# Kernel tuning notes

Measured on AMD Instinct MI355X. Metric: run time of the kernel, lower is better.

The kernel has to match this reference:

```python
import jax, jax.numpy as jnp
import numpy as np

S = 7               # grid size (config.S)
LAMBDA_COORD = 5.0  # YOLOv1 coordinate loss weight
LAMBDA_NOOBJ = 0.5  # YOLOv1 no-object confidence weight
BATCH = 16384


def _iou(a, b):
    """IoU of boxes in (cx, cy, w, h) format. a, b: [..., 4] -> [...]."""
    a_lt = a[..., 0:2] - a[..., 2:4] * 0.5
    a_rb = a[..., 0:2] + a[..., 2:4] * 0.5
    b_lt = b[..., 0:2] - b[..., 2:4] * 0.5
    b_rb = b[..., 0:2] + b[..., 2:4] * 0.5
    inter_wh = jnp.clip(jnp.minimum(a_rb, b_rb) - jnp.maximum(a_lt, b_lt), 0.0)
    inter = inter_wh[..., 0] * inter_wh[..., 1]
    area_a = a[..., 2] * a[..., 3]
    area_b = b[..., 2] * b[..., 3]
    return inter / (area_a + area_b - inter + 1e-10)


def setup_inputs() -> dict:
    key = jax.random.key(0)
    k1, k2, k3 = jax.random.split(key, 3)
    preds = jax.random.uniform(k1, (BATCH, S, S, 30), dtype=jnp.float32)
    labels = jax.random.uniform(k2, (BATCH, S, S, 30), dtype=jnp.float32)
    # objectness flag must be exactly 1.0 in object cells (labels[...,4]==1 check)
    conf = (jax.random.uniform(k3, (BATCH, S, S, 1)) > 0.7).astype(jnp.float32)
    labels = labels.at[..., 4:5].set(conf)
    labels = labels.at[..., 9:10].set(conf)
    return {"preds": preds, "labels": labels}


def _yolo_loss(preds, labels):
    obj = labels[..., 4]          # [B,S,S] 1.0 where an object is present
    noobj = 1.0 - obj
    gt = labels[..., 0:4]         # ground-truth box per cell
    p1 = preds[..., 0:4]          # bbox 1
    p2 = preds[..., 5:9]          # bbox 2

    iou1 = _iou(p1, gt)
    iou2 = _iou(p2, gt)
    resp1 = (iou1 > iou2).astype(preds.dtype)  # responsible-box selector
    r1 = resp1[..., None]

    resp_box = r1 * p1 + (1.0 - r1) * p2
    resp_conf = resp1 * preds[..., 4] + (1.0 - resp1) * preds[..., 9]
    other_conf = (1.0 - resp1) * preds[..., 4] + resp1 * preds[..., 9]
    resp_iou = jax.lax.stop_gradient(jnp.maximum(iou1, iou2))  # conf target

    om = obj[..., None]
    loss_xy = LAMBDA_COORD * jnp.sum(om * (resp_box[..., 0:2] - gt[..., 0:2]) ** 2)
    sqrt_p = jnp.sqrt(jnp.maximum(resp_box[..., 2:4], 1e-8))
    sqrt_g = jnp.sqrt(jnp.maximum(gt[..., 2:4], 1e-8))
    loss_wh = LAMBDA_COORD * jnp.sum(om * (sqrt_p - sqrt_g) ** 2)
    loss_obj = jnp.sum(obj * (resp_conf - resp_iou) ** 2)
    loss_noobj = LAMBDA_NOOBJ * (
        jnp.sum(noobj * (preds[..., 4] ** 2 + preds[..., 9] ** 2))
        + jnp.sum(obj * other_conf ** 2)
    )
    loss_cls = jnp.sum(om * (preds[..., 10:] - labels[..., 10:]) ** 2)

    total = loss_xy + loss_wh + loss_obj + loss_noobj + loss_cls
    return total / preds.shape[0]


def reference(preds, labels):
    return _yolo_loss(preds, labels)
```

## Files before the change

kernel.cpp:

```cpp
#include <hip/hip_runtime.h>

#define NCELLS (16384 * 7 * 7)
#define THREADS 256
#define TILE_CELLS 256
#define FLOATS_PER_TILE (TILE_CELLS * 30)
#define NTILES (NCELLS / TILE_CELLS)
#define GRID 256

__device__ __forceinline__ void gload16(const float* g, float* l) {
    __builtin_amdgcn_global_load_lds(
        (const __attribute__((address_space(1))) void*)g,
        (__attribute__((address_space(3))) void*)l, 16, 0, 0);
}

__device__ __forceinline__ void stage_tile(const float* __restrict__ preds,
                                           const float* __restrict__ labels,
                                           float* sp, float* sl,
                                           int tile, int wid, int lane) {
    size_t base = (size_t)tile * FLOATS_PER_TILE;
    #pragma unroll
    for (int k = 0; k < 15; ++k) {
        int c = wid * 15 + k;
        if (c < 30) {
            gload16(preds + base + (size_t)c * 256 + lane * 4, sp + c * 256);
        } else {
            int c2 = c - 30;
            gload16(labels + base + (size_t)c2 * 256 + lane * 4, sl + c2 * 256);
        }
    }
}

__device__ __forceinline__ float cell_loss(const float* p, const float* l) {
    float g_l = l[0] - l[2] * 0.5f, g_r = l[0] + l[2] * 0.5f;
    float g_t = l[1] - l[3] * 0.5f, g_b = l[1] + l[3] * 0.5f;
    float area_g = l[2] * l[3];

    float a_l = p[0] - p[2] * 0.5f, a_r = p[0] + p[2] * 0.5f;
    float a_t = p[1] - p[3] * 0.5f, a_b = p[1] + p[3] * 0.5f;
    float iw1 = fmaxf(fminf(a_r, g_r) - fmaxf(a_l, g_l), 0.0f);
    float ih1 = fmaxf(fminf(a_b, g_b) - fmaxf(a_t, g_t), 0.0f);
    float inter1 = iw1 * ih1;
    float iou1 = inter1 / (p[2] * p[3] + area_g - inter1 + 1e-10f);

    float b_l = p[5] - p[7] * 0.5f, b_r = p[5] + p[7] * 0.5f;
    float b_t = p[6] - p[8] * 0.5f, b_b = p[6] + p[8] * 0.5f;
    float iw2 = fmaxf(fminf(b_r, g_r) - fmaxf(b_l, g_l), 0.0f);
    float ih2 = fmaxf(fminf(b_b, g_b) - fmaxf(b_t, g_t), 0.0f);
    float inter2 = iw2 * ih2;
    float iou2 = inter2 / (p[7] * p[8] + area_g - inter2 + 1e-10f);

    bool r1 = iou1 > iou2;
    float rb0 = r1 ? p[0] : p[5];
    float rb1 = r1 ? p[1] : p[6];
    float rb2 = r1 ? p[2] : p[7];
    float rb3 = r1 ? p[3] : p[8];
    float rconf = r1 ? p[4] : p[9];
    float oconf = r1 ? p[9] : p[4];
    float riou = fmaxf(iou1, iou2);

    float dx = rb0 - l[0], dy = rb1 - l[1];
    float lxy = dx * dx + dy * dy;

    float spw = sqrtf(fmaxf(rb2, 1e-8f)), sgw = sqrtf(fmaxf(l[2], 1e-8f));
    float sph = sqrtf(fmaxf(rb3, 1e-8f)), sgh = sqrtf(fmaxf(l[3], 1e-8f));
    float dw = spw - sgw, dh = sph - sgh;
    float lwh = dw * dw + dh * dh;

    float dob = rconf - riou;

    float cls = 0.0f;
    #pragma unroll
    for (int c = 10; c < 30; ++c) {
        float d = p[c] - l[c];
        cls += d * d;
    }

    float obj = l[4];
    return obj * (5.0f * (lxy + lwh) + dob * dob + 0.5f * oconf * oconf + cls)
         + 0.5f * (1.0f - obj) * (p[4] * p[4] + p[9] * p[9]);
}

__device__ __forceinline__ float block_reduce(float acc) {
    #pragma unroll
    for (int off = 32; off > 0; off >>= 1) acc += __shfl_down(acc, off);
    __shared__ float s[THREADS / 64];
    int lane = threadIdx.x & 63, wid = threadIdx.x >> 6;
    if (lane == 0) s[wid] = acc;
    __syncthreads();
    float r = 0.0f;
    if (threadIdx.x == 0) {
        #pragma unroll
        for (int w = 0; w < THREADS / 64; ++w) r += s[w];
    }
    return r;
}

__global__ __launch_bounds__(THREADS, 1) void yolo_partial(
        const float* __restrict__ preds, const float* __restrict__ labels,
        float* __restrict__ out) {
    __shared__ float sp[2][FLOATS_PER_TILE];
    __shared__ float sl[2][FLOATS_PER_TILE];

    int lane = threadIdx.x & 63, wid = threadIdx.x >> 6;
    float acc = 0.0f;

    int tile = blockIdx.x;
    int buf = 0;
    if (tile < NTILES) stage_tile(preds, labels, sp[0], sl[0], tile, wid, lane);

    for (; tile < NTILES; tile += GRID, buf ^= 1) {
        asm volatile("s_waitcnt vmcnt(0)" ::: "memory");
        __syncthreads();
        int next = tile + GRID;
        if (next < NTILES)
            stage_tile(preds, labels, sp[buf ^ 1], sl[buf ^ 1], next, wid, lane);

        const float2* cp = (const float2*)(sp[buf] + threadIdx.x * 30);
        const float2* cl = (const float2*)(sl[buf] + threadIdx.x * 30);
        float p[30], l[30];
        #pragma unroll
        for (int i = 0; i < 15; ++i) {
            float2 v = cp[i]; p[2 * i] = v.x; p[2 * i + 1] = v.y;
        }
        #pragma unroll
        for (int i = 0; i < 15; ++i) {
            float2 v = cl[i]; l[2 * i] = v.x; l[2 * i + 1] = v.y;
        }
        acc += cell_loss(p, l);
    }

    float r = block_reduce(acc);
    if (threadIdx.x == 0) atomicAdd(out, r * (1.0f / 16384.0f));
}

extern "C" void kernel_launch(void* const* d_in, const int* in_sizes, int n_in,
                              void* d_out, int out_size, void* d_ws, size_t ws_size,
                              hipStream_t stream) {
    const float* preds  = (const float*)d_in[0];
    const float* labels = (const float*)d_in[1];
    float* out = (float*)d_out;

    hipMemsetAsync(out, 0, sizeof(float), stream);
    yolo_partial<<<GRID, THREADS, 0, stream>>>(preds, labels, out);
}
```

Measured before the change: 38.66 us.

## Use single-wave blocks with partial waitcnt pipelining and two-pass reduction

```diff
diff --git a/kernel.cpp b/kernel.cpp
--- a/kernel.cpp
+++ b/kernel.cpp
@@ -1,11 +1,11 @@
 #include <hip/hip_runtime.h>
 
 #define NCELLS (16384 * 7 * 7)
-#define THREADS 256
-#define TILE_CELLS 256
-#define FLOATS_PER_TILE (TILE_CELLS * 30)
-#define NTILES (NCELLS / TILE_CELLS)
-#define GRID 256
+#define TILE 128
+#define TFLOATS (TILE * 30)
+#define NTILES (NCELLS / TILE)
+#define GRID 512
+#define CHUNKS 15
 
 __device__ __forceinline__ void gload16(const float* g, float* l) {
     __builtin_amdgcn_global_load_lds(
@@ -16,18 +16,14 @@
 __device__ __forceinline__ void stage_tile(const float* __restrict__ preds,
                                            const float* __restrict__ labels,
                                            float* sp, float* sl,
-                                           int tile, int wid, int lane) {
-    size_t base = (size_t)tile * FLOATS_PER_TILE;
+                                           int tile, int lane) {
+    size_t base = (size_t)tile * TFLOATS;
     #pragma unroll
-    for (int k = 0; k < 15; ++k) {
-        int c = wid * 15 + k;
-        if (c < 30) {
-            gload16(preds + base + (size_t)c * 256 + lane * 4, sp + c * 256);
-        } else {
-            int c2 = c - 30;
-            gload16(labels + base + (size_t)c2 * 256 + lane * 4, sl + c2 * 256);
-        }
-    }
+    for (int c = 0; c < CHUNKS; ++c)
+        gload16(preds + base + c * 256 + lane * 4, sp + c * 256);
+    #pragma unroll
+    for (int c = 0; c < CHUNKS; ++c)
+        gload16(labels + base + c * 256 + lane * 4, sl + c * 256);
 }
 
 __device__ __forceinline__ float cell_loss(const float* p, const float* l) {
@@ -80,57 +76,65 @@
          + 0.5f * (1.0f - obj) * (p[4] * p[4] + p[9] * p[9]);
 }
 
-__device__ __forceinline__ float block_reduce(float acc) {
+__global__ __launch_bounds__(64) void yolo_partial(
+        const float* __restrict__ preds, const float* __restrict__ labels,
+        float* __restrict__ partials) {
+    __shared__ float S[2][2][TFLOATS];
+
+    int lane = threadIdx.x;
+    int t0 = blockIdx.x;
+    float acc = 0.0f;
+
+    stage_tile(preds, labels, S[0][0], S[0][1], t0, lane);
+
+    int buf = 0;
+    for (int t = t0; t < NTILES; t += GRID) {
+        int tn = t + GRID;
+        if (tn < NTILES) {
+            stage_tile(preds, labels, S[buf ^ 1][0], S[buf ^ 1][1], tn, lane);
+            asm volatile("s_waitcnt vmcnt(30)" ::: "memory");
+        } else {
+            asm volatile("s_waitcnt vmcnt(0)" ::: "memory");
+        }
+        __builtin_amdgcn_sched_barrier(0);
+
+        #pragma unroll
+        for (int h = 0; h < 2; ++h) {
+            int cell = h * 64 + lane;
+            const float2* cp = (const float2*)(S[buf][0] + cell * 30);
+            const float2* cl = (const float2*)(S[buf][1] + cell * 30);
+            float p[30], l[30];
+            #pragma unroll
+            for (int i = 0; i < 15; ++i) {
+                float2 v = cp[i]; p[2 * i] = v.x; p[2 * i + 1] = v.y;
+            }
+            #pragma unroll
+            for (int i = 0; i < 15; ++i) {
+                float2 v = cl[i]; l[2 * i] = v.x; l[2 * i + 1] = v.y;
+            }
+            acc += cell_loss(p, l);
+        }
+
+        buf ^= 1;
+    }
+
     #pragma unroll
     for (int off = 32; off > 0; off >>= 1) acc += __shfl_down(acc, off);
-    __shared__ float s[THREADS / 64];
+    if (lane == 0) partials[blockIdx.x] = acc;
+}
+
+__global__ __launch_bounds__(256) void yolo_final(
+        const float* __restrict__ partials, float* __restrict__ out) {
+    float acc = 0.0f;
+    for (int i = threadIdx.x; i < GRID; i += 256) acc += partials[i];
+    #pragma unroll
+    for (int off = 32; off > 0; off >>= 1) acc += __shfl_down(acc, off);
+    __shared__ float s[4];
     int lane = threadIdx.x & 63, wid = threadIdx.x >> 6;
     if (lane == 0) s[wid] = acc;
     __syncthreads();
-    float r = 0.0f;
-    if (threadIdx.x == 0) {
-        #pragma unroll
-        for (int w = 0; w < THREADS / 64; ++w) r += s[w];
-    }
-    return r;
-}
-
-__global__ __launch_bounds__(THREADS, 1) void yolo_partial(
-        const float* __restrict__ preds, const float* __restrict__ labels,
-        float* __restrict__ out) {
-    __shared__ float sp[2][FLOATS_PER_TILE];
-    __shared__ float sl[2][FLOATS_PER_TILE];
-
-    int lane = threadIdx.x & 63, wid = threadIdx.x >> 6;
-    float acc = 0.0f;
-
-    int tile = blockIdx.x;
-    int buf = 0;
-    if (tile < NTILES) stage_tile(preds, labels, sp[0], sl[0], tile, wid, lane);
-
-    for (; tile < NTILES; tile += GRID, buf ^= 1) {
-        asm volatile("s_waitcnt vmcnt(0)" ::: "memory");
-        __syncthreads();
-        int next = tile + GRID;
-        if (next < NTILES)
-            stage_tile(preds, labels, sp[buf ^ 1], sl[buf ^ 1], next, wid, lane);
-
-        const float2* cp = (const float2*)(sp[buf] + threadIdx.x * 30);
-        const float2* cl = (const float2*)(sl[buf] + threadIdx.x * 30);
-        float p[30], l[30];
-        #pragma unroll
-        for (int i = 0; i < 15; ++i) {
-            float2 v = cp[i]; p[2 * i] = v.x; p[2 * i + 1] = v.y;
-        }
-        #pragma unroll
-        for (int i = 0; i < 15; ++i) {
-            float2 v = cl[i]; l[2 * i] = v.x; l[2 * i + 1] = v.y;
-        }
-        acc += cell_loss(p, l);
-    }
-
-    float r = block_reduce(acc);
-    if (threadIdx.x == 0) atomicAdd(out, r * (1.0f / 16384.0f));
+    if (threadIdx.x == 0)
+        out[0] = (s[0] + s[1] + s[2] + s[3]) * (1.0f / 16384.0f);
 }
 
 extern "C" void kernel_launch(void* const* d_in, const int* in_sizes, int n_in,
@@ -139,7 +143,8 @@
     const float* preds  = (const float*)d_in[0];
     const float* labels = (const float*)d_in[1];
     float* out = (float*)d_out;
+    float* partials = (float*)d_ws;
 
-    hipMemsetAsync(out, 0, sizeof(float), stream);
-    yolo_partial<<<GRID, THREADS, 0, stream>>>(preds, labels, out);
+    yolo_partial<<<GRID, 64, 0, stream>>>(preds, labels, partials);
+    yolo_final<<<1, 256, 0, stream>>>(partials, out);
 }
```

New measurement: 39.05 us. No clear change (+1.0%).
